# Performance work log

Measured on AMD Instinct MI355X. Metric: run time of the kernel, lower is better.

The kernel has to match this reference:

```python
import jax, jax.numpy as jnp
import numpy as np

# static config (levels=4, CDA=False branch -> self_attn_4, scale=4, f=False)
SHAPES = [(80, 80), (40, 40), (20, 20), (10, 10)]
D = 256; NH = 8; NL = 4; NP = 4; DFF = 1024; DH = D // NH
L = sum(h * w for h, w in SHAPES)  # 8500
B = 1


def layer_norm(x, g, b, eps=1e-5):
    m = jnp.mean(x, axis=-1, keepdims=True)
    v = jnp.mean((x - m) ** 2, axis=-1, keepdims=True)
    return (x - m) * jax.lax.rsqrt(v + eps) * g + b


def ms_deform_attn_core(value, loc, attn):
    # value: [B, L, NH, DH]; loc: [B, Lq, NH, NL, NP, 2] in [0,1]; attn: [B, Lq, NH, NL, NP]
    Bq, Lq = loc.shape[0], loc.shape[1]
    out = jnp.zeros((Bq, NH, Lq, DH), value.dtype)
    start = 0
    for lvl, (Hl, Wl) in enumerate(SHAPES):
        v = value[:, start:start + Hl * Wl]          # [B, HW, NH, DH]
        start += Hl * Wl
        v = v.transpose(0, 2, 1, 3)                  # [B, NH, HW, DH]
        ll = loc[:, :, :, lvl]                       # [B, Lq, NH, NP, 2]
        # grid_sample semantics: align_corners=False, padding_mode='zeros'
        x = ll[..., 0] * Wl - 0.5
        y = ll[..., 1] * Hl - 0.5
        x0 = jnp.floor(x); y0 = jnp.floor(y)
        acc = jnp.zeros((Bq, NH, Lq, NP, DH), value.dtype)
        for dy in (0, 1):
            for dx in (0, 1):
                xi = x0 + dx; yi = y0 + dy
                w = (1.0 - jnp.abs(x - xi)) * (1.0 - jnp.abs(y - yi))  # [B,Lq,NH,NP]
                valid = (xi >= 0) & (xi < Wl) & (yi >= 0) & (yi < Hl)
                xi_c = jnp.clip(xi, 0, Wl - 1).astype(jnp.int32)
                yi_c = jnp.clip(yi, 0, Hl - 1).astype(jnp.int32)
                lin = (yi_c * Wl + xi_c).transpose(0, 2, 1, 3).reshape(Bq, NH, Lq * NP)
                g = jnp.take_along_axis(v, lin[..., None], axis=2).reshape(Bq, NH, Lq, NP, DH)
                wv = (w * valid.astype(w.dtype)).transpose(0, 2, 1, 3)[..., None]
                acc = acc + g * wv
        aw = attn[:, :, :, lvl].transpose(0, 2, 1, 3)[..., None]  # [B,NH,Lq,NP,1]
        out = out + jnp.sum(acc * aw, axis=3)
    return out.transpose(0, 2, 1, 3).reshape(Bq, Lq, NH * DH)


def setup_inputs():
    key = jax.random.key(0)
    ks = jax.random.split(key, 24)
    s = 0.02
    d = {}
    d['src'] = jax.random.normal(ks[0], (B, L, D), jnp.float32)
    d['pos'] = jax.random.normal(ks[1], (B, L, D), jnp.float32)
    d['reference_points'] = jax.random.uniform(ks[2], (B, L, NL, 2), jnp.float32)
    d['spatial_shapes'] = jnp.array(SHAPES, jnp.int32)
    d['level_start_index'] = jnp.array(np.cumsum([0] + [h * w for h, w in SHAPES[:-1]]), jnp.int32)
    d['scale'] = 4
    # MSDeformAttn params
    d['Wo'] = jax.random.normal(ks[3], (D, NH * NL * NP * 2), jnp.float32) * s
    d['bo'] = jax.random.normal(ks[4], (NH * NL * NP * 2,), jnp.float32) * s
    d['Wa'] = jax.random.normal(ks[5], (D, NH * NL * NP), jnp.float32) * s
    d['ba'] = jax.random.normal(ks[6], (NH * NL * NP,), jnp.float32) * s
    d['Wv'] = jax.random.normal(ks[7], (D, D), jnp.float32) * s
    d['bv'] = jnp.zeros((D,), jnp.float32)
    d['Wout'] = jax.random.normal(ks[8], (D, D), jnp.float32) * s
    d['bout'] = jnp.zeros((D,), jnp.float32)
    # FFN + LayerNorms
    d['W1'] = jax.random.normal(ks[9], (D, DFF), jnp.float32) * s
    d['b1'] = jnp.zeros((DFF,), jnp.float32)
    d['W2'] = jax.random.normal(ks[10], (DFF, D), jnp.float32) * s
    d['b2'] = jnp.zeros((D,), jnp.float32)
    d['g1'] = jnp.ones((D,), jnp.float32); d['be1'] = jnp.zeros((D,), jnp.float32)
    d['g2'] = jnp.ones((D,), jnp.float32); d['be2'] = jnp.zeros((D,), jnp.float32)
    return d


def reference(src, pos, reference_points, spatial_shapes, level_start_index, scale,
              Wo, bo, Wa, ba, Wv, bv, Wout, bout, W1, b1, W2, b2, g1, be1, g2, be2):
    Bq, Lq, _ = src.shape
    q = src + pos  # with_pos_embed
    # sampling offsets & attention weights (softmax over levels*points)
    off = (q @ Wo + bo).reshape(Bq, Lq, NH, NL, NP, 2)
    attn = jax.nn.softmax((q @ Wa + ba).reshape(Bq, Lq, NH, NL * NP), axis=-1)
    attn = attn.reshape(Bq, Lq, NH, NL, NP)
    value = (src @ Wv + bv).reshape(Bq, L, NH, DH)
    # offset normalizer is (W, H) per level
    normalizer = jnp.stack([spatial_shapes[:, 1], spatial_shapes[:, 0]], -1).astype(src.dtype)
    loc = reference_points[:, :, None, :, None, :] + off / normalizer[None, None, None, :, None, :]
    src2 = ms_deform_attn_core(value, loc, attn) @ Wout + bout
    # residual + norm1 (dropout = eval identity)
    x = layer_norm(src + src2, g1, be1)
    # FFN
    ffn = jax.nn.relu(x @ W1 + b1) @ W2 + b2
    x = layer_norm(x + ffn, g2, be2)
    return x
```

## Files before the change

kernel.cpp:

```cpp
#include <hip/hip_runtime.h>
#include <hip/hip_bf16.h>
#include <string.h>

#define D 256
#define NH 8
#define DH 32
#define NL 4
#define NP 4
#define DFF 1024
#define LTOT 8500

typedef __bf16 bf16x8 __attribute__((ext_vector_type(8)));
typedef float floatx4 __attribute__((ext_vector_type(4)));

__device__ inline unsigned bpack(float a, float b) {
    __hip_bfloat16 ha = __float2bfloat16(a), hb = __float2bfloat16(b);
    unsigned short ua, ub;
    memcpy(&ua, &ha, 2); memcpy(&ub, &hb, 2);
    return (unsigned)ua | ((unsigned)ub << 16);
}

__device__ inline void gload16(const void* g, void* l) {
    __builtin_amdgcn_global_load_lds((const __attribute__((address_space(1))) void*)g,
                                     (__attribute__((address_space(3))) void*)l,
                                     16, 0, 0);
}

__global__ void transpose_all(const float* W0, const float* W1_, const float* W2_,
                              const float* W3, const float* W4, const float* W5,
                              __hip_bfloat16* T0, __hip_bfloat16* T1, __hip_bfloat16* T2,
                              __hip_bfloat16* T3, __hip_bfloat16* T4, __hip_bfloat16* T5,
                              const float* src, const float* pos,
                              __hip_bfloat16* qb, __hip_bfloat16* srcb) {
    int id = blockIdx.x;
    if (id >= 736) {
        int idx = (id - 736) * 2048 + threadIdx.x * 8;
        if (idx < LTOT * 256) {
            float4 s0 = *(const float4*)(src + idx);
            float4 s1 = *(const float4*)(src + idx + 4);
            float4 p0 = *(const float4*)(pos + idx);
            float4 p1 = *(const float4*)(pos + idx + 4);
            uint4 us, uq;
            us.x = bpack(s0.x, s0.y); us.y = bpack(s0.z, s0.w);
            us.z = bpack(s1.x, s1.y); us.w = bpack(s1.z, s1.w);
            uq.x = bpack(s0.x + p0.x, s0.y + p0.y); uq.y = bpack(s0.z + p0.z, s0.w + p0.w);
            uq.z = bpack(s1.x + p1.x, s1.y + p1.y); uq.w = bpack(s1.z + p1.z, s1.w + p1.w);
            *(uint4*)(srcb + idx) = us;
            *(uint4*)(qb + idx)  = uq;
        }
        return;
    }
    const int cum[7] = {0, 64, 96, 160, 224, 480, 736};
    int mi = 0;
    while (id >= cum[mi + 1]) mi++;
    int lid = id - cum[mi];
    const float* W; __hip_bfloat16* T; int K, N;
    switch (mi) {
        case 0: W = W0; T = T0; K = 256;  N = 256;  break;
        case 1: W = W1_; T = T1; K = 256; N = 128;  break;
        case 2: W = W2_; T = T2; K = 256; N = 256;  break;
        case 3: W = W3; T = T3; K = 256;  N = 256;  break;
        case 4: W = W4; T = T4; K = 256;  N = 1024; break;
        default: W = W5; T = T5; K = 1024; N = 256; break;
    }
    int ntx = N >> 5;
    int n0 = (lid % ntx) * 32, k0 = (lid / ntx) * 32;
    __shared__ float t[32][33];
    int tx = threadIdx.x & 31, ty = threadIdx.x >> 5;
#pragma unroll
    for (int i = 0; i < 32; i += 8)
        t[ty + i][tx] = W[(size_t)(k0 + ty + i) * N + n0 + tx];
    __syncthreads();
#pragma unroll
    for (int i = 0; i < 32; i += 8)
        T[(size_t)(n0 + ty + i) * K + k0 + tx] = __float2bfloat16(t[tx][ty + i]);
}

__global__ __launch_bounds__(256) void gemm_t(
    const __hip_bfloat16* __restrict__ A, const __hip_bfloat16* __restrict__ BT,
    const float* __restrict__ bias, float* __restrict__ Cf, __hip_bfloat16* __restrict__ Cb,
    int M, int N, int K, int relu) {
    constexpr int BM = 64, BN = 64, BK = 64;
    __shared__ __align__(16) __hip_bfloat16 sA[BM * BK];
    __shared__ __align__(16) __hip_bfloat16 sB[BN * BK];

    int tid = threadIdx.x, wave = tid >> 6, lane = tid & 63;
    int m0 = blockIdx.y * BM, n0 = blockIdx.x * BN;
    int wm = (wave >> 1) * 32, wn = (wave & 1) * 32;

    floatx4 acc[2][2];
#pragma unroll
    for (int i = 0; i < 2; i++)
#pragma unroll
        for (int j = 0; j < 2; j++)
#pragma unroll
            for (int e = 0; e < 4; e++) acc[i][j][e] = 0.f;

    int lrow = lane & 15, swz = lrow & 7;
    int scol = ((lane & 7) ^ (lane >> 3)) << 3;

    const __hip_bfloat16* aP[2];
    const __hip_bfloat16* bP[2];
#pragma unroll
    for (int i = 0; i < 2; i++) {
        int ra = m0 + i * 32 + wave * 8 + (lane >> 3); if (ra >= M) ra = M - 1;
        aP[i] = A + (size_t)ra * K + scol;
        int rb = n0 + i * 32 + wave * 8 + (lane >> 3);
        bP[i] = BT + (size_t)rb * K + scol;
    }
    int dOff = wave * 1024 + lane * 16;

    for (int k0 = 0; k0 < K; k0 += BK) {
#pragma unroll
        for (int i = 0; i < 2; i++) gload16(aP[i] + k0, (char*)sA + i * 4096 + dOff);
#pragma unroll
        for (int i = 0; i < 2; i++) gload16(bP[i] + k0, (char*)sB + i * 4096 + dOff);
        __syncthreads();
#pragma unroll
        for (int kk = 0; kk < 2; kk++) {
            int co = (((kk << 2) + (lane >> 4)) ^ swz) << 3;
            bf16x8 af[2], bfr[2];
#pragma unroll
            for (int tm = 0; tm < 2; tm++)
                af[tm] = *(const bf16x8*)(&sA[(wm + tm * 16 + lrow) * BK + co]);
#pragma unroll
            for (int tn = 0; tn < 2; tn++)
                bfr[tn] = *(const bf16x8*)(&sB[(wn + tn * 16 + lrow) * BK + co]);
#pragma unroll
            for (int tm = 0; tm < 2; tm++)
#pragma unroll
                for (int tn = 0; tn < 2; tn++)
                    acc[tm][tn] = __builtin_amdgcn_mfma_f32_16x16x32_bf16(af[tm], bfr[tn], acc[tm][tn], 0, 0, 0);
        }
        __syncthreads();
    }

    int lcol = lane & 15, lr4 = (lane >> 4) * 4;
#pragma unroll
    for (int tm = 0; tm < 2; tm++) {
#pragma unroll
        for (int i = 0; i < 4; i++) {
            int row = m0 + wm + tm * 16 + lr4 + i;
            if (row < M) {
#pragma unroll
                for (int tn = 0; tn < 2; tn++) {
                    int col = n0 + wn + tn * 16 + lcol;
                    float v = acc[tm][tn][i] + bias[col];
                    if (relu) v = fmaxf(v, 0.f);
                    if (Cf) Cf[(size_t)row * N + col] = v;
                    if (Cb) Cb[(size_t)row * N + col] = __float2bfloat16(v);
                }
            }
        }
    }
}

__global__ __launch_bounds__(256) void proj2(
    const __hip_bfloat16* __restrict__ qb, const __hip_bfloat16* __restrict__ srcb,
    const __hip_bfloat16* __restrict__ WoT, const __hip_bfloat16* __restrict__ WaT,
    const __hip_bfloat16* __restrict__ WvT,
    const float* __restrict__ bo, const float* __restrict__ ba, const float* __restrict__ bv,
    float* __restrict__ locb, float* __restrict__ attnb, __hip_bfloat16* __restrict__ valb,
    int M) {
    constexpr int BM = 64, BN = 64, BK = 64, K = 256;
    __shared__ __align__(16) __hip_bfloat16 sA[BM * BK];
    __shared__ __align__(16) __hip_bfloat16 sB[BN * BK];

    int n0 = blockIdx.x * BN;
    int m0 = blockIdx.y * BM;

    const __hip_bfloat16* BT;
    const __hip_bfloat16* A;
    const float* bias;
    int ncol0, Nout;
    float* Cf; __hip_bfloat16* Cb;
    if (n0 < 256)      { A = qb;   BT = WoT; bias = bo; ncol0 = n0;       Nout = 256; Cf = locb;  Cb = nullptr; }
    else if (n0 < 384) { A = qb;   BT = WaT; bias = ba; ncol0 = n0 - 256; Nout = 128; Cf = attnb; Cb = nullptr; }
    else               { A = srcb; BT = WvT; bias = bv; ncol0 = n0 - 384; Nout = 256; Cf = nullptr; Cb = valb; }

    int tid = threadIdx.x, wave = tid >> 6, lane = tid & 63;
    int wm = (wave >> 1) * 32, wn = (wave & 1) * 32;

    floatx4 acc[2][2];
#pragma unroll
    for (int i = 0; i < 2; i++)
#pragma unroll
        for (int j = 0; j < 2; j++)
#pragma unroll
            for (int e = 0; e < 4; e++) acc[i][j][e] = 0.f;

    int lrow = lane & 15, swz = lrow & 7;
    int scol = ((lane & 7) ^ (lane >> 3)) << 3;

    const __hip_bfloat16* aP[2];
    const __hip_bfloat16* bP[2];
#pragma unroll
    for (int i = 0; i < 2; i++) {
        int ra = m0 + i * 32 + wave * 8 + (lane >> 3); if (ra >= M) ra = M - 1;
        aP[i] = A + (size_t)ra * K + scol;
        int rb = ncol0 + i * 32 + wave * 8 + (lane >> 3);
        bP[i] = BT + (size_t)rb * K + scol;
    }
    int dOff = wave * 1024 + lane * 16;

    for (int k0 = 0; k0 < K; k0 += BK) {
#pragma unroll
        for (int i = 0; i < 2; i++) gload16(aP[i] + k0, (char*)sA + i * 4096 + dOff);
#pragma unroll
        for (int i = 0; i < 2; i++) gload16(bP[i] + k0, (char*)sB + i * 4096 + dOff);
        __syncthreads();
#pragma unroll
        for (int kk = 0; kk < 2; kk++) {
            int co = (((kk << 2) + (lane >> 4)) ^ swz) << 3;
            bf16x8 af[2], bfr[2];
#pragma unroll
            for (int tm = 0; tm < 2; tm++)
                af[tm] = *(const bf16x8*)(&sA[(wm + tm * 16 + lrow) * BK + co]);
#pragma unroll
            for (int tn = 0; tn < 2; tn++)
                bfr[tn] = *(const bf16x8*)(&sB[(wn + tn * 16 + lrow) * BK + co]);
#pragma unroll
            for (int tm = 0; tm < 2; tm++)
#pragma unroll
                for (int tn = 0; tn < 2; tn++)
                    acc[tm][tn] = __builtin_amdgcn_mfma_f32_16x16x32_bf16(af[tm], bfr[tn], acc[tm][tn], 0, 0, 0);
        }
        __syncthreads();
    }

    int lcol = lane & 15, lr4 = (lane >> 4) * 4;
#pragma unroll
    for (int tm = 0; tm < 2; tm++) {
#pragma unroll
        for (int i = 0; i < 4; i++) {
            int row = m0 + wm + tm * 16 + lr4 + i;
            if (row < M) {
#pragma unroll
                for (int tn = 0; tn < 2; tn++) {
                    int col = ncol0 + wn + tn * 16 + lcol;
                    float v = acc[tm][tn][i] + bias[col];
                    if (Cf) Cf[(size_t)row * Nout + col] = v;
                    else    Cb[(size_t)row * Nout + col] = __float2bfloat16(v);
                }
            }
        }
    }
}

__global__ __launch_bounds__(256) void deform(const __hip_bfloat16* __restrict__ value,
                                              const float* __restrict__ locraw,
                                              const float* __restrict__ logits,
                                              const float* __restrict__ refp,
                                              __hip_bfloat16* __restrict__ out) {
    __shared__ float wS[4][8][16][4];
    __shared__ int   aS[4][8][16][4];
    int tid = threadIdx.x;
    int q0 = blockIdx.x * 4;

    {
        int sub = tid >> 6, h = (tid >> 3) & 7, t8 = tid & 7;
        int q = q0 + sub;
        const float* lg = logits + q * 128 + h * 16;
        float l0 = lg[t8], l1 = lg[t8 + 8];
        float mx = fmaxf(l0, l1);
#pragma unroll
        for (int m = 1; m < 8; m <<= 1) mx = fmaxf(mx, __shfl_xor(mx, m, 64));
        float e0 = __expf(l0 - mx), e1 = __expf(l1 - mx);
        float s = e0 + e1;
#pragma unroll
        for (int m = 1; m < 8; m <<= 1) s += __shfl_xor(s, m, 64);
        float inv = 1.f / s;

        const int starts[4] = {0, 6400, 8000, 8400};
#pragma unroll
        for (int j = 0; j < 2; j++) {
            int pp = t8 + 8 * j;
            float a = (j ? e1 : e0) * inv;
            int l = pp >> 2;
            int Wl = 80 >> l;
            float nv = (float)Wl;
            float rx = refp[q * 8 + l * 2 + 0];
            float ry = refp[q * 8 + l * 2 + 1];
            float lx = rx + locraw[q * 256 + h * 32 + pp * 2 + 0] / nv;
            float ly = ry + locraw[q * 256 + h * 32 + pp * 2 + 1] / nv;
            float x = lx * nv - 0.5f;
            float y = ly * nv - 0.5f;
            float x0f = floorf(x), y0f = floorf(y);
            float fx = x - x0f, fy = y - y0f;
            int x0 = (int)x0f, y0 = (int)y0f;
            float wts[4] = {(1.f - fx) * (1.f - fy), fx * (1.f - fy),
                            (1.f - fx) * fy,         fx * fy};
            int st = starts[l];
#pragma unroll
            for (int t = 0; t < 4; t++) {
                int xi = x0 + (t & 1), yi = y0 + (t >> 1);
                bool valid = (xi >= 0) & (xi < Wl) & (yi >= 0) & (yi < Wl);
                int xc = min(max(xi, 0), Wl - 1), yc = min(max(yi, 0), Wl - 1);
                wS[sub][h][pp][t] = valid ? wts[t] * a : 0.f;
                aS[sub][h][pp][t] = (st + yc * Wl + xc) * 512 + h * 64;
            }
        }
    }
    __syncthreads();

    int sub = tid >> 6, h = (tid >> 3) & 7, l8 = tid & 7;
    int q = q0 + sub;
    const char* vb = (const char*)value;
    int lo = l8 * 8;
    float a0 = 0.f, a1 = 0.f, a2 = 0.f, a3 = 0.f;
#pragma unroll
    for (int p = 0; p < 16; p++) {
        floatx4 w = *(const floatx4*)&wS[sub][h][p][0];
        int4 av = *(const int4*)&aS[sub][h][p][0];
#pragma unroll
        for (int t = 0; t < 4; t++) {
            int ad = (t == 0) ? av.x : (t == 1) ? av.y : (t == 2) ? av.z : av.w;
            uint2 u = *(const uint2*)(vb + ad + lo);
            float wt = w[t];
            a0 += wt * __uint_as_float(u.x << 16);
            a1 += wt * __uint_as_float(u.x & 0xffff0000u);
            a2 += wt * __uint_as_float(u.y << 16);
            a3 += wt * __uint_as_float(u.y & 0xffff0000u);
        }
    }
    uint2 o;
    o.x = bpack(a0, a1);
    o.y = bpack(a2, a3);
    *(uint2*)((char*)out + q * 512 + h * 64 + l8 * 8) = o;
}

__global__ __launch_bounds__(512) void gemm_ln(
    const __hip_bfloat16* __restrict__ A, const __hip_bfloat16* __restrict__ BT,
    const float* __restrict__ bias, const float* __restrict__ resid,
    const float* __restrict__ g, const float* __restrict__ be,
    float* __restrict__ outf, __hip_bfloat16* __restrict__ outb,
    int M, int K) {
    constexpr int BM = 16, BK = 64;
    __shared__ __align__(16) __hip_bfloat16 sA[BM * BK];
    __shared__ __align__(16) __hip_bfloat16 sB[256 * BK];
    __shared__ float psum[8][16], psq[8][16], mS[16], rS[16];

    int tid = threadIdx.x;
    int wave = tid >> 6, lane = tid & 63;
    int m0 = blockIdx.x * BM;

    floatx4 acc[2];
#pragma unroll
    for (int j = 0; j < 2; j++)
#pragma unroll
        for (int e = 0; e < 4; e++) acc[j][e] = 0.f;

    int lrow = lane & 15, swz = lrow & 7;

    int scolA = ((lane & 7) ^ (lane >> 3)) << 3;
    int grA = m0 + wave * 8 + (lane >> 3); if (grA >= M) grA = M - 1;
    const __hip_bfloat16* aP = A + (size_t)grA * K + scolA;

    int scolB = ((tid & 7) ^ ((tid >> 3) & 7)) << 3;
    const __hip_bfloat16* bP[4];
#pragma unroll
    for (int i = 0; i < 4; i++)
        bP[i] = BT + (size_t)(i * 64 + (tid >> 3)) * K + scolB;

    for (int k0 = 0; k0 < K; k0 += BK) {
        if (wave < 2) gload16(aP + k0, (char*)sA + wave * 1024 + lane * 16);
#pragma unroll
        for (int i = 0; i < 4; i++) gload16(bP[i] + k0, (char*)sB + i * 8192 + tid * 16);
        __syncthreads();
#pragma unroll
        for (int kk = 0; kk < 2; kk++) {
            int co = (((kk << 2) + (lane >> 4)) ^ swz) << 3;
            bf16x8 af, bfr[2];
            af = *(const bf16x8*)(&sA[lrow * BK + co]);
#pragma unroll
            for (int tn = 0; tn < 2; tn++)
                bfr[tn] = *(const bf16x8*)(&sB[(wave * 32 + tn * 16 + lrow) * BK + co]);
#pragma unroll
            for (int tn = 0; tn < 2; tn++)
                acc[tn] = __builtin_amdgcn_mfma_f32_16x16x32_bf16(af, bfr[tn], acc[tn], 0, 0, 0);
        }
        __syncthreads();
    }

    int lcol = lane & 15, quad = lane >> 4;
    float v[2][4];
#pragma unroll
    for (int i = 0; i < 4; i++) {
        int row = quad * 4 + i;
        int grow = m0 + row; if (grow >= M) grow = M - 1;
#pragma unroll
        for (int tn = 0; tn < 2; tn++) {
            int col = wave * 32 + tn * 16 + lcol;
            v[tn][i] = acc[tn][i] + bias[col] + resid[(size_t)grow * 256 + col];
        }
    }

#pragma unroll
    for (int i = 0; i < 4; i++) {
        float s = 0.f, s2 = 0.f;
#pragma unroll
        for (int tn = 0; tn < 2; tn++) { float x = v[tn][i]; s += x; s2 += x * x; }
#pragma unroll
        for (int m = 1; m < 16; m <<= 1) {
            s  += __shfl_xor(s, m, 64);
            s2 += __shfl_xor(s2, m, 64);
        }
        if (lcol == 0) {
            int row = quad * 4 + i;
            psum[wave][row] = s;
            psq[wave][row]  = s2;
        }
    }
    __syncthreads();
    if (tid < 16) {
        float s = 0.f, s2 = 0.f;
#pragma unroll
        for (int w = 0; w < 8; w++) { s += psum[w][tid]; s2 += psq[w][tid]; }
        float m = s * (1.f / 256.f);
        float var = fmaxf(s2 * (1.f / 256.f) - m * m, 0.f);
        mS[tid] = m;
        rS[tid] = rsqrtf(var + 1e-5f);
    }
    __syncthreads();

#pragma unroll
    for (int i = 0; i < 4; i++) {
        int row = quad * 4 + i;
        int grow = m0 + row;
        if (grow < M) {
            float m = mS[row], r = rS[row];
#pragma unroll
            for (int tn = 0; tn < 2; tn++) {
                int col = wave * 32 + tn * 16 + lcol;
                float o = (v[tn][i] - m) * r * g[col] + be[col];
                outf[(size_t)grow * 256 + col] = o;
                if (outb) outb[(size_t)grow * 256 + col] = __float2bfloat16(o);
            }
        }
    }
}

extern "C" void kernel_launch(void* const* d_in, const int* in_sizes, int n_in,
                              void* d_out, int out_size, void* d_ws, size_t ws_size,
                              hipStream_t stream) {
    const float* src  = (const float*)d_in[0];
    const float* pos  = (const float*)d_in[1];
    const float* refp = (const float*)d_in[2];
    const float* Wo   = (const float*)d_in[6];
    const float* bo   = (const float*)d_in[7];
    const float* Wa   = (const float*)d_in[8];
    const float* ba   = (const float*)d_in[9];
    const float* Wv   = (const float*)d_in[10];
    const float* bv   = (const float*)d_in[11];
    const float* Wout = (const float*)d_in[12];
    const float* bout = (const float*)d_in[13];
    const float* W1   = (const float*)d_in[14];
    const float* b1   = (const float*)d_in[15];
    const float* W2   = (const float*)d_in[16];
    const float* b2   = (const float*)d_in[17];
    const float* g1   = (const float*)d_in[18];
    const float* be1  = (const float*)d_in[19];
    const float* g2   = (const float*)d_in[20];
    const float* be2  = (const float*)d_in[21];
    float* out = (float*)d_out;
    char* ws = (char*)d_ws;

    __hip_bfloat16* WoT   = (__hip_bfloat16*)(ws + 0);
    __hip_bfloat16* WaT   = (__hip_bfloat16*)(ws + 131072);
    __hip_bfloat16* WvT   = (__hip_bfloat16*)(ws + 196608);
    __hip_bfloat16* WoutT = (__hip_bfloat16*)(ws + 327680);
    __hip_bfloat16* W1T   = (__hip_bfloat16*)(ws + 458752);
    __hip_bfloat16* W2T   = (__hip_bfloat16*)(ws + 983040);
    float*          locb  = (float*)(ws + 1507328);
    float*          attnb = (float*)(ws + 10211328);
    __hip_bfloat16* valb  = (__hip_bfloat16*)(ws + 14563328);
    __hip_bfloat16* aob   = (__hip_bfloat16*)(ws + 18915328);
    float*          x1    = (float*)(ws + 23267328);
    __hip_bfloat16* x1b   = (__hip_bfloat16*)(ws + 31971328);
    __hip_bfloat16* hb    = (__hip_bfloat16*)(ws + 36323328);
    __hip_bfloat16* qb    = (__hip_bfloat16*)(ws + 36323328);
    __hip_bfloat16* srcb  = (__hip_bfloat16*)(ws + 36323328 + 4352000);

    transpose_all<<<736 + 1063, 256, 0, stream>>>(Wo, Wa, Wv, Wout, W1, W2,
                                                  WoT, WaT, WvT, WoutT, W1T, W2T,
                                                  src, pos, qb, srcb);

    proj2<<<dim3(10, 133), 256, 0, stream>>>(qb, srcb, WoT, WaT, WvT, bo, ba, bv,
                                             locb, attnb, valb, LTOT);

    deform<<<2125, 256, 0, stream>>>(valb, locb, attnb, refp, aob);

    gemm_ln<<<532, 512, 0, stream>>>(aob, WoutT, bout, src, g1, be1, x1, x1b, LTOT, 256);

    gemm_t<<<dim3(16, 133), 256, 0, stream>>>(x1b, W1T, b1, nullptr, hb, LTOT, 1024, 256, 1);

    gemm_ln<<<532, 512, 0, stream>>>(hb, W2T, b2, x1, g2, be2, out, nullptr, LTOT, 1024);
}
```

Baseline: 197.0 us.

## Fuse deformable sampling into output-projection LN and fuse whole FFN per tile

The deformable attention gather now runs inside the output-projection+LayerNorm kernel, keeping the 16-row attention output tile in LDS instead of round-tripping through global memory. The FFN's two GEMMs are merged into one kernel that keeps the 16x1024 hidden activation in LDS, removing the hidden-buffer write and read and two launches. In exchange, each 16-row block now reloads the full W1 and W2 weights, only 532 blocks run with large LDS use, and the loops have no double-buffering, so latency hiding and occupancy may suffer.

```diff
diff --git a/kernel.cpp b/kernel.cpp
--- a/kernel.cpp
+++ b/kernel.cpp
@@ -76,85 +76,6 @@
         T[(size_t)(n0 + ty + i) * K + k0 + tx] = __float2bfloat16(t[tx][ty + i]);
 }
 
-__global__ __launch_bounds__(256) void gemm_t(
-    const __hip_bfloat16* __restrict__ A, const __hip_bfloat16* __restrict__ BT,
-    const float* __restrict__ bias, float* __restrict__ Cf, __hip_bfloat16* __restrict__ Cb,
-    int M, int N, int K, int relu) {
-    constexpr int BM = 64, BN = 64, BK = 64;
-    __shared__ __align__(16) __hip_bfloat16 sA[BM * BK];
-    __shared__ __align__(16) __hip_bfloat16 sB[BN * BK];
-
-    int tid = threadIdx.x, wave = tid >> 6, lane = tid & 63;
-    int m0 = blockIdx.y * BM, n0 = blockIdx.x * BN;
-    int wm = (wave >> 1) * 32, wn = (wave & 1) * 32;
-
-    floatx4 acc[2][2];
-#pragma unroll
-    for (int i = 0; i < 2; i++)
-#pragma unroll
-        for (int j = 0; j < 2; j++)
-#pragma unroll
-            for (int e = 0; e < 4; e++) acc[i][j][e] = 0.f;
-
-    int lrow = lane & 15, swz = lrow & 7;
-    int scol = ((lane & 7) ^ (lane >> 3)) << 3;
-
-    const __hip_bfloat16* aP[2];
-    const __hip_bfloat16* bP[2];
-#pragma unroll
-    for (int i = 0; i < 2; i++) {
-        int ra = m0 + i * 32 + wave * 8 + (lane >> 3); if (ra >= M) ra = M - 1;
-        aP[i] = A + (size_t)ra * K + scol;
-        int rb = n0 + i * 32 + wave * 8 + (lane >> 3);
-        bP[i] = BT + (size_t)rb * K + scol;
-    }
-    int dOff = wave * 1024 + lane * 16;
-
-    for (int k0 = 0; k0 < K; k0 += BK) {
-#pragma unroll
-        for (int i = 0; i < 2; i++) gload16(aP[i] + k0, (char*)sA + i * 4096 + dOff);
-#pragma unroll
-        for (int i = 0; i < 2; i++) gload16(bP[i] + k0, (char*)sB + i * 4096 + dOff);
-        __syncthreads();
-#pragma unroll
-        for (int kk = 0; kk < 2; kk++) {
-            int co = (((kk << 2) + (lane >> 4)) ^ swz) << 3;
-            bf16x8 af[2], bfr[2];
-#pragma unroll
-            for (int tm = 0; tm < 2; tm++)
-                af[tm] = *(const bf16x8*)(&sA[(wm + tm * 16 + lrow) * BK + co]);
-#pragma unroll
-            for (int tn = 0; tn < 2; tn++)
-                bfr[tn] = *(const bf16x8*)(&sB[(wn + tn * 16 + lrow) * BK + co]);
-#pragma unroll
-            for (int tm = 0; tm < 2; tm++)
-#pragma unroll
-                for (int tn = 0; tn < 2; tn++)
-                    acc[tm][tn] = __builtin_amdgcn_mfma_f32_16x16x32_bf16(af[tm], bfr[tn], acc[tm][tn], 0, 0, 0);
-        }
-        __syncthreads();
-    }
-
-    int lcol = lane & 15, lr4 = (lane >> 4) * 4;
-#pragma unroll
-    for (int tm = 0; tm < 2; tm++) {
-#pragma unroll
-        for (int i = 0; i < 4; i++) {
-            int row = m0 + wm + tm * 16 + lr4 + i;
-            if (row < M) {
-#pragma unroll
-                for (int tn = 0; tn < 2; tn++) {
-                    int col = n0 + wn + tn * 16 + lcol;
-                    float v = acc[tm][tn][i] + bias[col];
-                    if (relu) v = fmaxf(v, 0.f);
-                    if (Cf) Cf[(size_t)row * N + col] = v;
-                    if (Cb) Cb[(size_t)row * N + col] = __float2bfloat16(v);
-                }
-            }
-        }
-    }
-}
-
 __global__ __launch_bounds__(256) void proj2(
     const __hip_bfloat16* __restrict__ qb, const __hip_bfloat16* __restrict__ srcb,
     const __hip_bfloat16* __restrict__ WoT, const __hip_bfloat16* __restrict__ WaT,
@@ -247,134 +168,127 @@
     }
 }
 
-__global__ __launch_bounds__(256) void deform(const __hip_bfloat16* __restrict__ value,
-                                              const float* __restrict__ locraw,
-                                              const float* __restrict__ logits,
-                                              const float* __restrict__ refp,
-                                              __hip_bfloat16* __restrict__ out) {
-    __shared__ float wS[4][8][16][4];
-    __shared__ int   aS[4][8][16][4];
-    int tid = threadIdx.x;
-    int q0 = blockIdx.x * 4;
-
-    {
-        int sub = tid >> 6, h = (tid >> 3) & 7, t8 = tid & 7;
-        int q = q0 + sub;
-        const float* lg = logits + q * 128 + h * 16;
-        float l0 = lg[t8], l1 = lg[t8 + 8];
-        float mx = fmaxf(l0, l1);
-#pragma unroll
-        for (int m = 1; m < 8; m <<= 1) mx = fmaxf(mx, __shfl_xor(mx, m, 64));
-        float e0 = __expf(l0 - mx), e1 = __expf(l1 - mx);
-        float s = e0 + e1;
-#pragma unroll
-        for (int m = 1; m < 8; m <<= 1) s += __shfl_xor(s, m, 64);
-        float inv = 1.f / s;
-
-        const int starts[4] = {0, 6400, 8000, 8400};
-#pragma unroll
-        for (int j = 0; j < 2; j++) {
-            int pp = t8 + 8 * j;
-            float a = (j ? e1 : e0) * inv;
-            int l = pp >> 2;
-            int Wl = 80 >> l;
-            float nv = (float)Wl;
-            float rx = refp[q * 8 + l * 2 + 0];
-            float ry = refp[q * 8 + l * 2 + 1];
-            float lx = rx + locraw[q * 256 + h * 32 + pp * 2 + 0] / nv;
-            float ly = ry + locraw[q * 256 + h * 32 + pp * 2 + 1] / nv;
-            float x = lx * nv - 0.5f;
-            float y = ly * nv - 0.5f;
-            float x0f = floorf(x), y0f = floorf(y);
-            float fx = x - x0f, fy = y - y0f;
-            int x0 = (int)x0f, y0 = (int)y0f;
-            float wts[4] = {(1.f - fx) * (1.f - fy), fx * (1.f - fy),
-                            (1.f - fx) * fy,         fx * fy};
-            int st = starts[l];
-#pragma unroll
-            for (int t = 0; t < 4; t++) {
-                int xi = x0 + (t & 1), yi = y0 + (t >> 1);
-                bool valid = (xi >= 0) & (xi < Wl) & (yi >= 0) & (yi < Wl);
-                int xc = min(max(xi, 0), Wl - 1), yc = min(max(yi, 0), Wl - 1);
-                wS[sub][h][pp][t] = valid ? wts[t] * a : 0.f;
-                aS[sub][h][pp][t] = (st + yc * Wl + xc) * 512 + h * 64;
-            }
-        }
-    }
-    __syncthreads();
-
-    int sub = tid >> 6, h = (tid >> 3) & 7, l8 = tid & 7;
-    int q = q0 + sub;
-    const char* vb = (const char*)value;
-    int lo = l8 * 8;
-    float a0 = 0.f, a1 = 0.f, a2 = 0.f, a3 = 0.f;
-#pragma unroll
-    for (int p = 0; p < 16; p++) {
-        floatx4 w = *(const floatx4*)&wS[sub][h][p][0];
-        int4 av = *(const int4*)&aS[sub][h][p][0];
-#pragma unroll
-        for (int t = 0; t < 4; t++) {
-            int ad = (t == 0) ? av.x : (t == 1) ? av.y : (t == 2) ? av.z : av.w;
-            uint2 u = *(const uint2*)(vb + ad + lo);
-            float wt = w[t];
-            a0 += wt * __uint_as_float(u.x << 16);
-            a1 += wt * __uint_as_float(u.x & 0xffff0000u);
-            a2 += wt * __uint_as_float(u.y << 16);
-            a3 += wt * __uint_as_float(u.y & 0xffff0000u);
-        }
-    }
-    uint2 o;
-    o.x = bpack(a0, a1);
-    o.y = bpack(a2, a3);
-    *(uint2*)((char*)out + q * 512 + h * 64 + l8 * 8) = o;
-}
-
-__global__ __launch_bounds__(512) void gemm_ln(
-    const __hip_bfloat16* __restrict__ A, const __hip_bfloat16* __restrict__ BT,
-    const float* __restrict__ bias, const float* __restrict__ resid,
+__global__ __launch_bounds__(512) void deform_ln(
+    const __hip_bfloat16* __restrict__ value,
+    const float* __restrict__ locraw,
+    const float* __restrict__ logits,
+    const float* __restrict__ refp,
+    const __hip_bfloat16* __restrict__ BT,
+    const float* __restrict__ bias,
+    const float* __restrict__ resid,
     const float* __restrict__ g, const float* __restrict__ be,
     float* __restrict__ outf, __hip_bfloat16* __restrict__ outb,
-    int M, int K) {
-    constexpr int BM = 16, BK = 64;
-    __shared__ __align__(16) __hip_bfloat16 sA[BM * BK];
-    __shared__ __align__(16) __hip_bfloat16 sB[256 * BK];
+    int M) {
+    __shared__ float wS[8][8][16][4];
+    __shared__ int   aS[8][8][16][4];
+    __shared__ __align__(16) __hip_bfloat16 aobL[16][264];
+    __shared__ __align__(16) __hip_bfloat16 sB[256 * 64];
     __shared__ float psum[8][16], psq[8][16], mS[16], rS[16];
 
-    int tid = threadIdx.x;
-    int wave = tid >> 6, lane = tid & 63;
-    int m0 = blockIdx.x * BM;
-
-    floatx4 acc[2];
-#pragma unroll
-    for (int j = 0; j < 2; j++)
-#pragma unroll
-        for (int e = 0; e < 4; e++) acc[j][e] = 0.f;
-
-    int lrow = lane & 15, swz = lrow & 7;
-
-    int scolA = ((lane & 7) ^ (lane >> 3)) << 3;
-    int grA = m0 + wave * 8 + (lane >> 3); if (grA >= M) grA = M - 1;
-    const __hip_bfloat16* aP = A + (size_t)grA * K + scolA;
-
+    int tid = threadIdx.x, wave = tid >> 6, lane = tid & 63;
+    int m0 = blockIdx.x * 16;
+
+    for (int r = 0; r < 2; r++) {
+        int sub = tid >> 6, h = (tid >> 3) & 7, t8 = tid & 7;
+        int q = m0 + r * 8 + sub; if (q >= M) q = M - 1;
+        {
+            const float* lg = logits + q * 128 + h * 16;
+            float l0 = lg[t8], l1 = lg[t8 + 8];
+            float mx = fmaxf(l0, l1);
+#pragma unroll
+            for (int m = 1; m < 8; m <<= 1) mx = fmaxf(mx, __shfl_xor(mx, m, 64));
+            float e0 = __expf(l0 - mx), e1 = __expf(l1 - mx);
+            float s = e0 + e1;
+#pragma unroll
+            for (int m = 1; m < 8; m <<= 1) s += __shfl_xor(s, m, 64);
+            float inv = 1.f / s;
+
+            const int starts[4] = {0, 6400, 8000, 8400};
+#pragma unroll
+            for (int j = 0; j < 2; j++) {
+                int pp = t8 + 8 * j;
+                float a = (j ? e1 : e0) * inv;
+                int l = pp >> 2;
+                int Wl = 80 >> l;
+                float nv = (float)Wl;
+                float rx = refp[q * 8 + l * 2 + 0];
+                float ry = refp[q * 8 + l * 2 + 1];
+                float lx = rx + locraw[q * 256 + h * 32 + pp * 2 + 0] / nv;
+                float ly = ry + locraw[q * 256 + h * 32 + pp * 2 + 1] / nv;
+                float x = lx * nv - 0.5f;
+                float y = ly * nv - 0.5f;
+                float x0f = floorf(x), y0f = floorf(y);
+                float fx = x - x0f, fy = y - y0f;
+                int x0 = (int)x0f, y0 = (int)y0f;
+                float wts[4] = {(1.f - fx) * (1.f - fy), fx * (1.f - fy),
+                                (1.f - fx) * fy,         fx * fy};
+                int st = starts[l];
+#pragma unroll
+                for (int t = 0; t < 4; t++) {
+                    int xi = x0 + (t & 1), yi = y0 + (t >> 1);
+                    bool valid = (xi >= 0) & (xi < Wl) & (yi >= 0) & (yi < Wl);
+                    int xc = min(max(xi, 0), Wl - 1), yc = min(max(yi, 0), Wl - 1);
+                    wS[sub][h][pp][t] = valid ? wts[t] * a : 0.f;
+                    aS[sub][h][pp][t] = (st + yc * Wl + xc) * 512 + h * 64;
+                }
+            }
+        }
+        __syncthreads();
+
+        {
+            int l8 = tid & 7;
+            const char* vb = (const char*)value;
+            int lo = l8 * 8;
+            float a0 = 0.f, a1 = 0.f, a2 = 0.f, a3 = 0.f;
+#pragma unroll
+            for (int p = 0; p < 16; p++) {
+                floatx4 w = *(const floatx4*)&wS[sub][h][p][0];
+                int4 av = *(const int4*)&aS[sub][h][p][0];
+#pragma unroll
+                for (int t = 0; t < 4; t++) {
+                    int ad = (t == 0) ? av.x : (t == 1) ? av.y : (t == 2) ? av.z : av.w;
+                    uint2 u = *(const uint2*)(vb + ad + lo);
+                    float wt = w[t];
+                    a0 += wt * __uint_as_float(u.x << 16);
+                    a1 += wt * __uint_as_float(u.x & 0xffff0000u);
+                    a2 += wt * __uint_as_float(u.y << 16);
+                    a3 += wt * __uint_as_float(u.y & 0xffff0000u);
+                }
+            }
+            uint2 o;
+            o.x = bpack(a0, a1);
+            o.y = bpack(a2, a3);
+            int lr = r * 8 + sub;
+            *(uint2*)((char*)&aobL[0][0] + lr * 528 + h * 64 + l8 * 8) = o;
+        }
+        __syncthreads();
+    }
+
+    int lrow = lane & 15, swz = lrow & 7, q2 = lane >> 4;
     int scolB = ((tid & 7) ^ ((tid >> 3) & 7)) << 3;
     const __hip_bfloat16* bP[4];
 #pragma unroll
     for (int i = 0; i < 4; i++)
-        bP[i] = BT + (size_t)(i * 64 + (tid >> 3)) * K + scolB;
-
-    for (int k0 = 0; k0 < K; k0 += BK) {
-        if (wave < 2) gload16(aP + k0, (char*)sA + wave * 1024 + lane * 16);
-#pragma unroll
-        for (int i = 0; i < 4; i++) gload16(bP[i] + k0, (char*)sB + i * 8192 + tid * 16);
+        bP[i] = BT + (size_t)(i * 64 + (tid >> 3)) * 256 + scolB;
+
+    floatx4 acc[2];
+#pragma unroll
+    for (int j = 0; j < 2; j++)
+#pragma unroll
+        for (int e = 0; e < 4; e++) acc[j][e] = 0.f;
+
+    for (int t = 0; t < 4; t++) {
+#pragma unroll
+        for (int i = 0; i < 4; i++) gload16(bP[i] + t * 64, (char*)sB + i * 8192 + tid * 16);
         __syncthreads();
 #pragma unroll
         for (int kk = 0; kk < 2; kk++) {
-            int co = (((kk << 2) + (lane >> 4)) ^ swz) << 3;
-            bf16x8 af, bfr[2];
-            af = *(const bf16x8*)(&sA[lrow * BK + co]);
+            int co = (((kk << 2) + q2) ^ swz) << 3;
+            bf16x8 af = *(const bf16x8*)(&aobL[lrow][t * 64 + kk * 32 + q2 * 8]);
+            bf16x8 bfr[2];
 #pragma unroll
             for (int tn = 0; tn < 2; tn++)
-                bfr[tn] = *(const bf16x8*)(&sB[(wave * 32 + tn * 16 + lrow) * BK + co]);
+                bfr[tn] = *(const bf16x8*)(&sB[(wave * 32 + tn * 16 + lrow) * 64 + co]);
 #pragma unroll
             for (int tn = 0; tn < 2; tn++)
                 acc[tn] = __builtin_amdgcn_mfma_f32_16x16x32_bf16(af, bfr[tn], acc[tn], 0, 0, 0);
@@ -428,13 +342,170 @@
         int row = quad * 4 + i;
         int grow = m0 + row;
         if (grow < M) {
-            float m = mS[row], r = rS[row];
+            float m = mS[row], rr = rS[row];
 #pragma unroll
             for (int tn = 0; tn < 2; tn++) {
                 int col = wave * 32 + tn * 16 + lcol;
-                float o = (v[tn][i] - m) * r * g[col] + be[col];
+                float o = (v[tn][i] - m) * rr * g[col] + be[col];
                 outf[(size_t)grow * 256 + col] = o;
-                if (outb) outb[(size_t)grow * 256 + col] = __float2bfloat16(o);
+                outb[(size_t)grow * 256 + col] = __float2bfloat16(o);
+            }
+        }
+    }
+}
+
+__global__ __launch_bounds__(512) void ffn(
+    const __hip_bfloat16* __restrict__ A,
+    const __hip_bfloat16* __restrict__ W1T,
+    const float* __restrict__ b1,
+    const __hip_bfloat16* __restrict__ W2T,
+    const float* __restrict__ b2,
+    const float* __restrict__ resid,
+    const float* __restrict__ g, const float* __restrict__ be,
+    float* __restrict__ outf, int M) {
+    __shared__ __align__(16) __hip_bfloat16 sAx[16 * 256];
+    __shared__ __align__(16) __hip_bfloat16 H[16 * 1032];
+    __shared__ __align__(16) __hip_bfloat16 sB[256 * 64];
+    __shared__ float psum[8][16], psq[8][16], mS[16], rS[16];
+
+    int tid = threadIdx.x, wave = tid >> 6, lane = tid & 63;
+    int m0 = blockIdx.x * 16;
+    int lrow = lane & 15, swz = lrow & 7, q2 = lane >> 4;
+    int quad = lane >> 4, lcol = lane & 15;
+    int swzA = (lrow & 7) << 3;
+
+    {
+        int rr = tid >> 5, cc = tid & 31;
+        int gr = m0 + rr; if (gr >= M) gr = M - 1;
+        int colel = (cc * 8) ^ ((rr & 7) << 3);
+        gload16(A + (size_t)gr * 256 + colel, (char*)sAx + tid * 16);
+    }
+
+    int scolB = ((tid & 7) ^ ((tid >> 3) & 7)) << 3;
+
+    for (int c = 0; c < 4; c++) {
+        const __hip_bfloat16* bP[4];
+#pragma unroll
+        for (int i = 0; i < 4; i++)
+            bP[i] = W1T + (size_t)(c * 256 + i * 64 + (tid >> 3)) * 256 + scolB;
+
+        floatx4 acc[2];
+#pragma unroll
+        for (int j = 0; j < 2; j++)
+#pragma unroll
+            for (int e = 0; e < 4; e++) acc[j][e] = 0.f;
+
+        for (int t = 0; t < 4; t++) {
+#pragma unroll
+            for (int i = 0; i < 4; i++) gload16(bP[i] + t * 64, (char*)sB + i * 8192 + tid * 16);
+            __syncthreads();
+#pragma unroll
+            for (int kk = 0; kk < 2; kk++) {
+                int co = (((kk << 2) + q2) ^ swz) << 3;
+                bf16x8 af = *(const bf16x8*)(&sAx[lrow * 256 + ((t * 64 + kk * 32 + q2 * 8) ^ swzA)]);
+                bf16x8 bfr[2];
+#pragma unroll
+                for (int tn = 0; tn < 2; tn++)
+                    bfr[tn] = *(const bf16x8*)(&sB[(wave * 32 + tn * 16 + lrow) * 64 + co]);
+#pragma unroll
+                for (int tn = 0; tn < 2; tn++)
+                    acc[tn] = __builtin_amdgcn_mfma_f32_16x16x32_bf16(af, bfr[tn], acc[tn], 0, 0, 0);
+            }
+            __syncthreads();
+        }
+
+#pragma unroll
+        for (int i = 0; i < 4; i++) {
+            int row = quad * 4 + i;
+#pragma unroll
+            for (int tn = 0; tn < 2; tn++) {
+                int col = c * 256 + wave * 32 + tn * 16 + lcol;
+                float v = acc[tn][i] + b1[col];
+                H[row * 1032 + col] = __float2bfloat16(fmaxf(v, 0.f));
+            }
+        }
+    }
+
+    const __hip_bfloat16* bP2[4];
+#pragma unroll
+    for (int i = 0; i < 4; i++)
+        bP2[i] = W2T + (size_t)(i * 64 + (tid >> 3)) * 1024 + scolB;
+
+    floatx4 acc2[2];
+#pragma unroll
+    for (int j = 0; j < 2; j++)
+#pragma unroll
+        for (int e = 0; e < 4; e++) acc2[j][e] = 0.f;
+
+    for (int t = 0; t < 16; t++) {
+#pragma unroll
+        for (int i = 0; i < 4; i++) gload16(bP2[i] + t * 64, (char*)sB + i * 8192 + tid * 16);
+        __syncthreads();
+#pragma unroll
+        for (int kk = 0; kk < 2; kk++) {
+            int co = (((kk << 2) + q2) ^ swz) << 3;
+            bf16x8 af = *(const bf16x8*)(&H[lrow * 1032 + t * 64 + kk * 32 + q2 * 8]);
+            bf16x8 bfr[2];
+#pragma unroll
+            for (int tn = 0; tn < 2; tn++)
+                bfr[tn] = *(const bf16x8*)(&sB[(wave * 32 + tn * 16 + lrow) * 64 + co]);
+#pragma unroll
+            for (int tn = 0; tn < 2; tn++)
+                acc2[tn] = __builtin_amdgcn_mfma_f32_16x16x32_bf16(af, bfr[tn], acc2[tn], 0, 0, 0);
+        }
+        __syncthreads();
+    }
+
+    float v[2][4];
+#pragma unroll
+    for (int i = 0; i < 4; i++) {
+        int row = quad * 4 + i;
+        int grow = m0 + row; if (grow >= M) grow = M - 1;
+#pragma unroll
+        for (int tn = 0; tn < 2; tn++) {
+            int col = wave * 32 + tn * 16 + lcol;
+            v[tn][i] = acc2[tn][i] + b2[col] + resid[(size_t)grow * 256 + col];
+        }
+    }
+
+#pragma unroll
+    for (int i = 0; i < 4; i++) {
+        float s = 0.f, s2 = 0.f;
+#pragma unroll
+        for (int tn = 0; tn < 2; tn++) { float x = v[tn][i]; s += x; s2 += x * x; }
+#pragma unroll
+        for (int m = 1; m < 16; m <<= 1) {
+            s  += __shfl_xor(s, m, 64);
+            s2 += __shfl_xor(s2, m, 64);
+        }
+        if (lcol == 0) {
+            int row = quad * 4 + i;
+            psum[wave][row] = s;
+            psq[wave][row]  = s2;
+        }
+    }
+    __syncthreads();
+    if (tid < 16) {
+        float s = 0.f, s2 = 0.f;
+#pragma unroll
+        for (int w = 0; w < 8; w++) { s += psum[w][tid]; s2 += psq[w][tid]; }
+        float m = s * (1.f / 256.f);
+        float var = fmaxf(s2 * (1.f / 256.f) - m * m, 0.f);
+        mS[tid] = m;
+        rS[tid] = rsqrtf(var + 1e-5f);
+    }
+    __syncthreads();
+
+#pragma unroll
+    for (int i = 0; i < 4; i++) {
+        int row = quad * 4 + i;
+        int grow = m0 + row;
+        if (grow < M) {
+            float m = mS[row], rr = rS[row];
+#pragma unroll
+            for (int tn = 0; tn < 2; tn++) {
+                int col = wave * 32 + tn * 16 + lcol;
+                outf[(size_t)grow * 256 + col] = (v[tn][i] - m) * rr * g[col] + be[col];
             }
         }
     }
@@ -474,10 +545,8 @@
     float*          locb  = (float*)(ws + 1507328);
     float*          attnb = (float*)(ws + 10211328);
     __hip_bfloat16* valb  = (__hip_bfloat16*)(ws + 14563328);
-    __hip_bfloat16* aob   = (__hip_bfloat16*)(ws + 18915328);
     float*          x1    = (float*)(ws + 23267328);
     __hip_bfloat16* x1b   = (__hip_bfloat16*)(ws + 31971328);
-    __hip_bfloat16* hb    = (__hip_bfloat16*)(ws + 36323328);
     __hip_bfloat16* qb    = (__hip_bfloat16*)(ws + 36323328);
     __hip_bfloat16* srcb  = (__hip_bfloat16*)(ws + 36323328 + 4352000);
 
@@ -488,11 +557,8 @@
     proj2<<<dim3(10, 133), 256, 0, stream>>>(qb, srcb, WoT, WaT, WvT, bo, ba, bv,
                                              locb, attnb, valb, LTOT);
 
-    deform<<<2125, 256, 0, stream>>>(valb, locb, attnb, refp, aob);
-
-    gemm_ln<<<532, 512, 0, stream>>>(aob, WoutT, bout, src, g1, be1, x1, x1b, LTOT, 256);
-
-    gemm_t<<<dim3(16, 133), 256, 0, stream>>>(x1b, W1T, b1, nullptr, hb, LTOT, 1024, 256, 1);
-
-    gemm_ln<<<532, 512, 0, stream>>>(hb, W2T, b2, x1, g2, be2, out, nullptr, LTOT, 1024);
-}
+    deform_ln<<<532, 512, 0, stream>>>(valb, locb, attnb, refp, WoutT, bout,
+                                       src, g1, be1, x1, x1b, LTOT);
+
+    ffn<<<532, 512, 0, stream>>>(x1b, W1T, b1, W2T, b2, x1, g2, be2, out, LTOT);
+}
```

Result: slower. 218.1 us (+10.7%).
